# Optimization experiments

Measured on AMD Instinct MI355X. Metric: run time of the kernel, lower is better.

The kernel has to match this reference:

```python
import jax, jax.numpy as jnp
import numpy as np

# ---- config (mirrors CoInHead init + TARGET_ASSIGNER_CONFIG) ----
PCR0, PCR1 = -51.2, -51.2          # point_cloud_range x/y min
VX, VY = 0.05, 0.05                # voxel_size x/y
STRIDE = 4                         # FEATURE_MAP_STRIDE
FW, FH = 512, 512                  # feature_map_size [x, y] = grid/stride
NUM_CLASSES = 10
NUM_MAX_OBJS = 500
OVERLAP = 0.1                      # GAUSSIAN_OVERLAP
MIN_RADIUS = 2
RMAX = 16                          # static cap on radius (covers all synthetic boxes)
K = 2 * RMAX + 1                   # fixed gaussian patch size
EPS = float(np.finfo(np.float32).eps)
BATCH = 16


def _gaussian_radius(height, width, min_overlap):
    # faithful to centernet_utils.gaussian_radius (OpenPCDet)
    b1 = height + width
    c1 = width * height * (1.0 - min_overlap) / (1.0 + min_overlap)
    sq1 = jnp.sqrt(jnp.maximum(b1 * b1 - 4.0 * c1, 0.0))
    r1 = (b1 + sq1) / 2.0

    b2 = 2.0 * (height + width)
    c2 = (1.0 - min_overlap) * width * height
    sq2 = jnp.sqrt(jnp.maximum(b2 * b2 - 16.0 * c2, 0.0))
    r2 = (b2 + sq2) / 2.0

    a3 = 4.0 * min_overlap
    b3 = -2.0 * min_overlap * (height + width)
    c3 = (min_overlap - 1.0) * width * height
    sq3 = jnp.sqrt(jnp.maximum(b3 * b3 - 4.0 * a3 * c3, 0.0))
    r3 = (b3 + sq3) / (2.0 * a3)
    return jnp.minimum(jnp.minimum(r1, r2), r3)


def setup_inputs() -> dict:
    key = jax.random.key(0)
    ks = jax.random.split(key, 8)
    B, M = BATCH, NUM_MAX_OBJS
    x = jax.random.uniform(ks[0], (B, M), minval=-50.0, maxval=50.0)
    y = jax.random.uniform(ks[1], (B, M), minval=-50.0, maxval=50.0)
    z = jax.random.uniform(ks[2], (B, M), minval=-2.0, maxval=1.0)
    dx = jax.random.uniform(ks[3], (B, M), minval=0.5, maxval=6.0)
    dy = jax.random.uniform(ks[4], (B, M), minval=0.5, maxval=6.0)
    dz = jax.random.uniform(ks[5], (B, M), minval=0.5, maxval=3.0)
    heading = jax.random.uniform(ks[6], (B, M), minval=-np.pi, maxval=np.pi)
    cls = jax.random.randint(ks[7], (B, M), 1, NUM_CLASSES + 1).astype(jnp.float32)
    gt_boxes = jnp.stack([x, y, z, dx, dy, dz, heading, cls], axis=-1).astype(jnp.float32)
    return {"gt_boxes": gt_boxes}


def reference(gt_boxes):
    # vectorized assign_target_of_single_head over (batch, objects)
    B, M, _ = gt_boxes.shape
    f32 = jnp.float32
    x, y, z = gt_boxes[..., 0], gt_boxes[..., 1], gt_boxes[..., 2]
    dx, dy, dz = gt_boxes[..., 3], gt_boxes[..., 4], gt_boxes[..., 5]
    heading = gt_boxes[..., 6]
    cls = (gt_boxes[..., 7] - 1.0).astype(jnp.int32)          # 0-based class id

    coord_x = jnp.clip((x - PCR0) / VX / STRIDE, 0.0, FW - 0.5)
    coord_y = jnp.clip((y - PCR1) / VY / STRIDE, 0.0, FH - 0.5)
    cxi = coord_x.astype(jnp.int32)
    cyi = coord_y.astype(jnp.int32)

    dxf = dx / VX / STRIDE
    dyf = dy / VY / STRIDE
    radius = _gaussian_radius(dxf, dyf, OVERLAP)
    radius = jnp.clip(radius.astype(jnp.int32), MIN_RADIUS, RMAX)  # (B, M)

    valid = (dxf > 0) & (dyf > 0) & (cxi >= 0) & (cxi <= FW) & (cyi >= 0) & (cyi <= FH)

    # fixed KxK gaussian patch centered on the integer center
    off = jnp.arange(K, dtype=jnp.int32) - RMAX
    oi = off[:, None]                                   # (K,1) row offset
    oj = off[None, :]                                   # (1,K) col offset
    sigma = (2.0 * radius.astype(f32) + 1.0) / 6.0      # diameter/6
    d2 = (oi * oi + oj * oj).astype(f32)                # (K,K)
    g = jnp.exp(-d2[None, None] / (2.0 * sigma[..., None, None] ** 2))  # (B,M,K,K)
    g = jnp.where(g < EPS, 0.0, g)                      # gaussian_2d eps truncation

    r_bm = radius[..., None, None]
    within = (jnp.abs(oi)[None, None] <= r_bm) & (jnp.abs(oj)[None, None] <= r_bm)
    yy = cyi[..., None, None] + oi[None, None]          # (B,M,K,K)
    xx = cxi[..., None, None] + oj[None, None]
    inb = (yy >= 0) & (yy < FH) & (xx >= 0) & (xx < FW)
    vals = jnp.where(valid[..., None, None] & within & inb, g, 0.0)

    b_idx = jnp.arange(B, dtype=jnp.int32)[:, None, None, None]
    c_idx = jnp.clip(cls, 0, NUM_CLASSES - 1)[..., None, None]
    heatmap = jnp.zeros((B, NUM_CLASSES, FH, FW), f32).at[
        b_idx, c_idx, jnp.clip(yy, 0, FH - 1), jnp.clip(xx, 0, FW - 1)
    ].max(vals)

    inds = jnp.where(valid, cyi * FW + cxi, 0).astype(jnp.int64)
    mask = valid.astype(jnp.int64)

    vf = valid.astype(f32)[..., None]
    ret_boxes = jnp.stack([
        coord_x - cxi.astype(f32),
        coord_y - cyi.astype(f32),
        z,
        jnp.log(jnp.maximum(dx, 1e-12)),
        jnp.log(jnp.maximum(dy, 1e-12)),
        jnp.log(jnp.maximum(dz, 1e-12)),
        jnp.cos(heading),
        jnp.sin(heading),
    ], axis=-1) * vf                                     # (B,M,8)

    return heatmap, ret_boxes, inds, mask
```

## Files before the change

### kernel.cpp

```cpp
#include <hip/hip_runtime.h>
#include <hip/hip_bf16.h>

#define PCR0   (-51.2f)
#define PCR1   (-51.2f)
#define VX_    (0.05f)
#define VY_    (0.05f)
#define STRIDE_ 4.0f
#define FW_    512
#define FH_    512
#define NCLS   10
#define NOBJ   500
#define OVERLAP_ 0.1f
#define MINRAD 2
#define RMAX_  16
#define BATCH_ 16
#define EPS_   1.1920928955078125e-07f

#define HEATMAP_ELEMS  (BATCH_ * NCLS * FH_ * FW_)
#define RETBOX_OFF     HEATMAP_ELEMS
#define RETBOX_ELEMS   (BATCH_ * NOBJ * 8)
#define INDS_OFF       (RETBOX_OFF + RETBOX_ELEMS)
#define MASK_OFF       (INDS_OFF + BATCH_ * NOBJ)

#define BAND_  32
#define NBAND  (FH_ / BAND_)
#define NBINS  (BATCH_ * NCLS * NBAND)
#define CAPB   NOBJ

#define CNT_BYTES   (NBINS * 4)
#define REC_OFF     CNT_BYTES
#define REC_BYTES   (BATCH_ * NOBJ * 16)
#define LIST_OFF    (REC_OFF + REC_BYTES)
#define LIST_BYTES  ((size_t)NBINS * CAPB * 4)
#define WS_NEEDED   (LIST_OFF + LIST_BYTES)

__device__ __forceinline__ void obj_params(const float* g8,
        float& coord_x, float& coord_y, int& cxi, int& cyi,
        int& radius, bool& valid)
{
    const float x = g8[0], y = g8[1];
    const float dx = g8[3], dy = g8[4];

    coord_x = fminf(fmaxf((x - PCR0) / VX_ / STRIDE_, 0.f), (float)FW_ - 0.5f);
    coord_y = fminf(fmaxf((y - PCR1) / VY_ / STRIDE_, 0.f), (float)FH_ - 0.5f);
    cxi = (int)coord_x;
    cyi = (int)coord_y;

    float dxf = dx / VX_ / STRIDE_;
    float dyf = dy / VY_ / STRIDE_;

    const float h = dxf, w = dyf, o = OVERLAP_;
    float b1 = h + w;
    float c1 = w * h * (1.f - o) / (1.f + o);
    float r1 = (b1 + sqrtf(fmaxf(b1 * b1 - 4.f * c1, 0.f))) * 0.5f;
    float b2 = 2.f * (h + w);
    float c2 = (1.f - o) * w * h;
    float r2 = (b2 + sqrtf(fmaxf(b2 * b2 - 16.f * c2, 0.f))) * 0.5f;
    float a3 = 4.f * o;
    float b3 = -2.f * o * (h + w);
    float c3 = (o - 1.f) * w * h;
    float r3 = (b3 + sqrtf(fmaxf(b3 * b3 - 4.f * a3 * c3, 0.f))) / (2.f * a3);
    float radf = fminf(fminf(r1, r2), r3);
    radius = (int)radf;
    radius = min(max(radius, MINRAD), RMAX_);

    valid = (dxf > 0.f) && (dyf > 0.f) &&
            (cxi >= 0) && (cxi <= FW_) && (cyi >= 0) && (cyi <= FH_);
}

__global__ void phaseA(const float* __restrict__ gt, float* __restrict__ out,
                       int* __restrict__ cnt, int* __restrict__ lists,
                       int4* __restrict__ recs)
{
    int obj = blockIdx.x * blockDim.x + threadIdx.x;
    if (obj >= BATCH_ * NOBJ) return;
    int b = obj / NOBJ;

    const float* g8 = gt + (size_t)obj * 8;
    float coord_x, coord_y; int cxi, cyi, radius; bool valid;
    obj_params(g8, coord_x, coord_y, cxi, cyi, radius, valid);

    const float z = g8[2], dx = g8[3], dy = g8[4], dz = g8[5];
    const float hd = g8[6], clsf = g8[7];

    float vf = valid ? 1.f : 0.f;
    float* rb = out + RETBOX_OFF + (size_t)obj * 8;
    rb[0] = (coord_x - (float)cxi) * vf;
    rb[1] = (coord_y - (float)cyi) * vf;
    rb[2] = z * vf;
    rb[3] = logf(fmaxf(dx, 1e-12f)) * vf;
    rb[4] = logf(fmaxf(dy, 1e-12f)) * vf;
    rb[5] = logf(fmaxf(dz, 1e-12f)) * vf;
    rb[6] = cosf(hd) * vf;
    rb[7] = sinf(hd) * vf;
    out[INDS_OFF + obj] = valid ? (float)(cyi * FW_ + cxi) : 0.f;
    out[MASK_OFF + obj] = vf;

    int c = min(max((int)(clsf - 1.0f), 0), NCLS - 1);
    float sigma = (2.f * (float)radius + 1.f) / 6.f;
    float negInv = -1.0f / (2.f * sigma * sigma);

    int4 r;
    r.x = cxi; r.y = cyi; r.z = radius; r.w = __float_as_int(negInv);
    recs[obj] = r;

    if (!valid) return;

    int ty0 = max(cyi - radius, 0) >> 5;
    int ty1 = min(cyi + radius, FH_ - 1) >> 5;
    int binbase = (b * NCLS + c) * NBAND;
    for (int ty = ty0; ty <= ty1; ++ty) {
        int bin = binbase + ty;
        int pos = atomicAdd(&cnt[bin], 1);
        if (pos < CAPB) lists[(size_t)bin * CAPB + pos] = obj;
    }
}

__global__ __launch_bounds__(512) void phaseB(
        float* __restrict__ out,
        const int* __restrict__ cnt, const int* __restrict__ lists,
        const int4* __restrict__ recs)
{
    const int bid = blockIdx.x;
    const int t   = threadIdx.x;
    const int col0  = (t & 127) << 2;
    const int r0    = __builtin_amdgcn_readfirstlane(t >> 7);
    const int wbase = __builtin_amdgcn_readfirstlane(((t >> 6) & 1) << 8);
    const int y0    = (bid & (NBAND - 1)) << 5;

    float acc[8][4];
    #pragma unroll
    for (int s = 0; s < 8; ++s) {
        acc[s][0] = 0.f; acc[s][1] = 0.f; acc[s][2] = 0.f; acc[s][3] = 0.f;
    }

    int n = cnt[bid]; if (n > CAPB) n = CAPB;
    const int* lst = lists + (size_t)bid * CAPB;

    for (int it = 0; it < n; ++it) {
        int o = __builtin_amdgcn_readfirstlane(lst[it]);
        int4 r = recs[o];
        int cxi   = __builtin_amdgcn_readfirstlane(r.x);
        int cyi   = __builtin_amdgcn_readfirstlane(r.y);
        int rad   = __builtin_amdgcn_readfirstlane(r.z);
        float negInv = __int_as_float(__builtin_amdgcn_readfirstlane(r.w));

        if (cxi + rad < wbase || cxi - rad > wbase + 255) continue;

        float cexp[4]; bool colin[4];
        #pragma unroll
        for (int k = 0; k < 4; ++k) {
            int rx = col0 + k - cxi;
            colin[k] = (rx >= -rad) && (rx <= rad);
            cexp[k]  = __expf((float)(rx * rx) * negInv);
        }

        #pragma unroll
        for (int s = 0; s < 8; ++s) {
            int ry = y0 + 4 * s + r0 - cyi;
            if (ry < -rad || ry > rad) continue;
            float rexp = __expf((float)(ry * ry) * negInv);
            #pragma unroll
            for (int k = 0; k < 4; ++k) {
                float g = rexp * cexp[k];
                bool ok = colin[k] && (g >= EPS_);
                acc[s][k] = ok ? fmaxf(acc[s][k], g) : acc[s][k];
            }
        }
    }

    float4* out4 = (float4*)(out + (size_t)bid * (BAND_ * FW_));
    #pragma unroll
    for (int s = 0; s < 8; ++s)
        out4[s * 512 + t] = make_float4(acc[s][0], acc[s][1], acc[s][2], acc[s][3]);
}

__global__ void zero_heatmap(float4* __restrict__ hm4, int n4) {
    int idx = blockIdx.x * blockDim.x + threadIdx.x;
    int stride = gridDim.x * blockDim.x;
    float4 z = make_float4(0.f, 0.f, 0.f, 0.f);
    for (int i = idx; i < n4; i += stride) hm4[i] = z;
}

__global__ __launch_bounds__(256) void paint_objects(
        const float* __restrict__ gt, float* __restrict__ out)
{
    const int obj = blockIdx.x;
    const int b   = obj / NOBJ;
    const float* g8 = gt + (size_t)obj * 8;

    float coord_x, coord_y; int cxi, cyi, radius; bool valid;
    obj_params(g8, coord_x, coord_y, cxi, cyi, radius, valid);

    const float z = g8[2], dx = g8[3], dy = g8[4], dz = g8[5];
    const float hd = g8[6], clsf = g8[7];

    if (threadIdx.x == 0) {
        float vf = valid ? 1.f : 0.f;
        float* rb = out + RETBOX_OFF + (size_t)obj * 8;
        rb[0] = (coord_x - (float)cxi) * vf;
        rb[1] = (coord_y - (float)cyi) * vf;
        rb[2] = z * vf;
        rb[3] = logf(fmaxf(dx, 1e-12f)) * vf;
        rb[4] = logf(fmaxf(dy, 1e-12f)) * vf;
        rb[5] = logf(fmaxf(dz, 1e-12f)) * vf;
        rb[6] = cosf(hd) * vf;
        rb[7] = sinf(hd) * vf;
        out[INDS_OFF + obj] = valid ? (float)(cyi * FW_ + cxi) : 0.f;
        out[MASK_OFF + obj] = vf;
    }
    if (!valid) return;

    float sigma = (2.f * (float)radius + 1.f) / 6.f;
    float denom = 2.f * sigma * sigma;
    int side = 2 * radius + 1;
    int npos = side * side;
    int c = min(max((int)(clsf - 1.0f), 0), NCLS - 1);
    float* hm = out + ((size_t)b * NCLS + c) * (size_t)(FH_ * FW_);

    for (int idx = threadIdx.x; idx < npos; idx += blockDim.x) {
        int i = idx / side - radius;
        int j = idx % side - radius;
        float d2 = (float)(i * i + j * j);
        float gv = expf(-d2 / denom);
        if (gv < EPS_) continue;
        int yy = cyi + i;
        int xx = cxi + j;
        if (yy < 0 || yy >= FH_ || xx < 0 || xx >= FW_) continue;
        atomicMax((int*)(hm + (size_t)yy * FW_ + xx), __float_as_int(gv));
    }
}

extern "C" void kernel_launch(void* const* d_in, const int* in_sizes, int n_in,
                              void* d_out, int out_size, void* d_ws, size_t ws_size,
                              hipStream_t stream) {
    const float* gt = (const float*)d_in[0];
    float* out = (float*)d_out;

    if (ws_size >= WS_NEEDED) {
        int* cnt     = (int*)d_ws;
        int4* recs   = (int4*)((char*)d_ws + REC_OFF);
        int* lists   = (int*)((char*)d_ws + LIST_OFF);

        hipMemsetAsync(cnt, 0, CNT_BYTES, stream);

        phaseA<<<(BATCH_ * NOBJ + 255) / 256, 256, 0, stream>>>(gt, out, cnt, lists, recs);
        phaseB<<<NBINS, 512, 0, stream>>>(out, cnt, lists, recs);
    } else {
        int n4 = HEATMAP_ELEMS / 4;
        zero_heatmap<<<4096, 256, 0, stream>>>((float4*)out, n4);
        paint_objects<<<BATCH_ * NOBJ, 256, 0, stream>>>(gt, out);
    }
}
```

Baseline: 170.7 us.

## Fuse binning and band painting into one kernel with shared-memory object lists

Replaces the memset, global binning kernel and band-painting kernel with a single kernel. Each block recomputes object parameters for its batch and filters the objects belonging to its class and band into a shared-memory list, then paints the band. This removes two launches, the global atomics and the workspace list traffic. In exchange every block redoes the per-object parameter math for all 500 objects, and the order of objects in the shared list is nondeterministic, which does not change the max result.

```diff
diff --git a/kernel.cpp b/kernel.cpp
--- a/kernel.cpp
+++ b/kernel.cpp
@@ -25,14 +25,6 @@
 #define BAND_  32
 #define NBAND  (FH_ / BAND_)
 #define NBINS  (BATCH_ * NCLS * NBAND)
-#define CAPB   NOBJ
-
-#define CNT_BYTES   (NBINS * 4)
-#define REC_OFF     CNT_BYTES
-#define REC_BYTES   (BATCH_ * NOBJ * 16)
-#define LIST_OFF    (REC_OFF + REC_BYTES)
-#define LIST_BYTES  ((size_t)NBINS * CAPB * 4)
-#define WS_NEEDED   (LIST_OFF + LIST_BYTES)
 
 __device__ __forceinline__ void obj_params(const float* g8,
         float& coord_x, float& coord_y, int& cxi, int& cyi,
@@ -68,65 +60,60 @@
             (cxi >= 0) && (cxi <= FW_) && (cyi >= 0) && (cyi <= FH_);
 }
 
-__global__ void phaseA(const float* __restrict__ gt, float* __restrict__ out,
-                       int* __restrict__ cnt, int* __restrict__ lists,
-                       int4* __restrict__ recs)
+__global__ __launch_bounds__(512) void fused(
+        const float* __restrict__ gt, float* __restrict__ out)
 {
-    int obj = blockIdx.x * blockDim.x + threadIdx.x;
-    if (obj >= BATCH_ * NOBJ) return;
-    int b = obj / NOBJ;
+    const int bid  = blockIdx.x;
+    const int b    = bid / (NCLS * NBAND);
+    const int rem  = bid - b * (NCLS * NBAND);
+    const int myc  = rem >> 4;
+    const int band = rem & (NBAND - 1);
+    const int y0   = band << 5;
 
-    const float* g8 = gt + (size_t)obj * 8;
-    float coord_x, coord_y; int cxi, cyi, radius; bool valid;
-    obj_params(g8, coord_x, coord_y, cxi, cyi, radius, valid);
+    __shared__ int  s_cnt;
+    __shared__ int4 s_rec[NOBJ];
 
-    const float z = g8[2], dx = g8[3], dy = g8[4], dz = g8[5];
-    const float hd = g8[6], clsf = g8[7];
+    if (threadIdx.x == 0) s_cnt = 0;
+    __syncthreads();
 
-    float vf = valid ? 1.f : 0.f;
-    float* rb = out + RETBOX_OFF + (size_t)obj * 8;
-    rb[0] = (coord_x - (float)cxi) * vf;
-    rb[1] = (coord_y - (float)cyi) * vf;
-    rb[2] = z * vf;
-    rb[3] = logf(fmaxf(dx, 1e-12f)) * vf;
-    rb[4] = logf(fmaxf(dy, 1e-12f)) * vf;
-    rb[5] = logf(fmaxf(dz, 1e-12f)) * vf;
-    rb[6] = cosf(hd) * vf;
-    rb[7] = sinf(hd) * vf;
-    out[INDS_OFF + obj] = valid ? (float)(cyi * FW_ + cxi) : 0.f;
-    out[MASK_OFF + obj] = vf;
+    const int t = threadIdx.x;
+    if (t < NOBJ) {
+        const int obj = b * NOBJ + t;
+        const float* g8 = gt + (size_t)obj * 8;
+        float coord_x, coord_y; int cxi, cyi, radius; bool valid;
+        obj_params(g8, coord_x, coord_y, cxi, cyi, radius, valid);
+        int c = min(max((int)(g8[7] - 1.0f), 0), NCLS - 1);
 
-    int c = min(max((int)(clsf - 1.0f), 0), NCLS - 1);
-    float sigma = (2.f * (float)radius + 1.f) / 6.f;
-    float negInv = -1.0f / (2.f * sigma * sigma);
+        if (myc == 0 && band == 0) {
+            const float z = g8[2], dx = g8[3], dy = g8[4], dz = g8[5];
+            const float hd = g8[6];
+            float vf = valid ? 1.f : 0.f;
+            float* rb = out + RETBOX_OFF + (size_t)obj * 8;
+            rb[0] = (coord_x - (float)cxi) * vf;
+            rb[1] = (coord_y - (float)cyi) * vf;
+            rb[2] = z * vf;
+            rb[3] = logf(fmaxf(dx, 1e-12f)) * vf;
+            rb[4] = logf(fmaxf(dy, 1e-12f)) * vf;
+            rb[5] = logf(fmaxf(dz, 1e-12f)) * vf;
+            rb[6] = cosf(hd) * vf;
+            rb[7] = sinf(hd) * vf;
+            out[INDS_OFF + obj] = valid ? (float)(cyi * FW_ + cxi) : 0.f;
+            out[MASK_OFF + obj] = vf;
+        }
 
-    int4 r;
-    r.x = cxi; r.y = cyi; r.z = radius; r.w = __float_as_int(negInv);
-    recs[obj] = r;
+        if (valid && c == myc &&
+            (cyi + radius >= y0) && (cyi - radius <= y0 + BAND_ - 1)) {
+            float sigma = (2.f * (float)radius + 1.f) / 6.f;
+            float negInv = -1.0f / (2.f * sigma * sigma);
+            int pos = atomicAdd(&s_cnt, 1);
+            s_rec[pos] = make_int4(cxi, cyi, radius, __float_as_int(negInv));
+        }
+    }
+    __syncthreads();
 
-    if (!valid) return;
-
-    int ty0 = max(cyi - radius, 0) >> 5;
-    int ty1 = min(cyi + radius, FH_ - 1) >> 5;
-    int binbase = (b * NCLS + c) * NBAND;
-    for (int ty = ty0; ty <= ty1; ++ty) {
-        int bin = binbase + ty;
-        int pos = atomicAdd(&cnt[bin], 1);
-        if (pos < CAPB) lists[(size_t)bin * CAPB + pos] = obj;
-    }
-}
-
-__global__ __launch_bounds__(512) void phaseB(
-        float* __restrict__ out,
-        const int* __restrict__ cnt, const int* __restrict__ lists,
-        const int4* __restrict__ recs)
-{
-    const int bid = blockIdx.x;
-    const int t   = threadIdx.x;
     const int col0  = (t & 127) << 2;
     const int r0    = __builtin_amdgcn_readfirstlane(t >> 7);
     const int wbase = __builtin_amdgcn_readfirstlane(((t >> 6) & 1) << 8);
-    const int y0    = (bid & (NBAND - 1)) << 5;
 
     float acc[8][4];
     #pragma unroll
@@ -134,12 +121,9 @@
         acc[s][0] = 0.f; acc[s][1] = 0.f; acc[s][2] = 0.f; acc[s][3] = 0.f;
     }
 
-    int n = cnt[bid]; if (n > CAPB) n = CAPB;
-    const int* lst = lists + (size_t)bid * CAPB;
-
+    const int n = s_cnt;
     for (int it = 0; it < n; ++it) {
-        int o = __builtin_amdgcn_readfirstlane(lst[it]);
-        int4 r = recs[o];
+        int4 r = s_rec[it];
         int cxi   = __builtin_amdgcn_readfirstlane(r.x);
         int cyi   = __builtin_amdgcn_readfirstlane(r.y);
         int rad   = __builtin_amdgcn_readfirstlane(r.z);
@@ -175,80 +159,10 @@
         out4[s * 512 + t] = make_float4(acc[s][0], acc[s][1], acc[s][2], acc[s][3]);
 }
 
-__global__ void zero_heatmap(float4* __restrict__ hm4, int n4) {
-    int idx = blockIdx.x * blockDim.x + threadIdx.x;
-    int stride = gridDim.x * blockDim.x;
-    float4 z = make_float4(0.f, 0.f, 0.f, 0.f);
-    for (int i = idx; i < n4; i += stride) hm4[i] = z;
-}
-
-__global__ __launch_bounds__(256) void paint_objects(
-        const float* __restrict__ gt, float* __restrict__ out)
-{
-    const int obj = blockIdx.x;
-    const int b   = obj / NOBJ;
-    const float* g8 = gt + (size_t)obj * 8;
-
-    float coord_x, coord_y; int cxi, cyi, radius; bool valid;
-    obj_params(g8, coord_x, coord_y, cxi, cyi, radius, valid);
-
-    const float z = g8[2], dx = g8[3], dy = g8[4], dz = g8[5];
-    const float hd = g8[6], clsf = g8[7];
-
-    if (threadIdx.x == 0) {
-        float vf = valid ? 1.f : 0.f;
-        float* rb = out + RETBOX_OFF + (size_t)obj * 8;
-        rb[0] = (coord_x - (float)cxi) * vf;
-        rb[1] = (coord_y - (float)cyi) * vf;
-        rb[2] = z * vf;
-        rb[3] = logf(fmaxf(dx, 1e-12f)) * vf;
-        rb[4] = logf(fmaxf(dy, 1e-12f)) * vf;
-        rb[5] = logf(fmaxf(dz, 1e-12f)) * vf;
-        rb[6] = cosf(hd) * vf;
-        rb[7] = sinf(hd) * vf;
-        out[INDS_OFF + obj] = valid ? (float)(cyi * FW_ + cxi) : 0.f;
-        out[MASK_OFF + obj] = vf;
-    }
-    if (!valid) return;
-
-    float sigma = (2.f * (float)radius + 1.f) / 6.f;
-    float denom = 2.f * sigma * sigma;
-    int side = 2 * radius + 1;
-    int npos = side * side;
-    int c = min(max((int)(clsf - 1.0f), 0), NCLS - 1);
-    float* hm = out + ((size_t)b * NCLS + c) * (size_t)(FH_ * FW_);
-
-    for (int idx = threadIdx.x; idx < npos; idx += blockDim.x) {
-        int i = idx / side - radius;
-        int j = idx % side - radius;
-        float d2 = (float)(i * i + j * j);
-        float gv = expf(-d2 / denom);
-        if (gv < EPS_) continue;
-        int yy = cyi + i;
-        int xx = cxi + j;
-        if (yy < 0 || yy >= FH_ || xx < 0 || xx >= FW_) continue;
-        atomicMax((int*)(hm + (size_t)yy * FW_ + xx), __float_as_int(gv));
-    }
-}
-
 extern "C" void kernel_launch(void* const* d_in, const int* in_sizes, int n_in,
                               void* d_out, int out_size, void* d_ws, size_t ws_size,
                               hipStream_t stream) {
     const float* gt = (const float*)d_in[0];
     float* out = (float*)d_out;
-
-    if (ws_size >= WS_NEEDED) {
-        int* cnt     = (int*)d_ws;
-        int4* recs   = (int4*)((char*)d_ws + REC_OFF);
-        int* lists   = (int*)((char*)d_ws + LIST_OFF);
-
-        hipMemsetAsync(cnt, 0, CNT_BYTES, stream);
-
-        phaseA<<<(BATCH_ * NOBJ + 255) / 256, 256, 0, stream>>>(gt, out, cnt, lists, recs);
-        phaseB<<<NBINS, 512, 0, stream>>>(out, cnt, lists, recs);
-    } else {
-        int n4 = HEATMAP_ELEMS / 4;
-        zero_heatmap<<<4096, 256, 0, stream>>>((float4*)out, n4);
-        paint_objects<<<BATCH_ * NOBJ, 256, 0, stream>>>(gt, out);
-    }
+    fused<<<NBINS, 512, 0, stream>>>(gt, out);
 }
```

After: 168.2 us. About the same (-1.5%).
